# Kernel optimization log

Hardware: AMD Instinct MI355X
Metric: run time of the kernel (lower is better)

## Reference

```python
import jax, jax.numpy as jnp
import numpy as np

N = 50000       # nodes
E = 800000      # edges
IN = 256        # input channels
H = 4           # heads
C = 64          # hidden channels per head
NEG_SLOPE = 0.2 # PyG GATConv default LeakyReLU slope
EPS = 1e-16


def setup_inputs() -> dict:
    key = jax.random.key(0)
    k_x, k_e, k_w, k_as, k_ad = jax.random.split(key, 5)
    x = jax.random.normal(k_x, (N, IN), dtype=jnp.float32)
    edge_index = jax.random.randint(k_e, (2, E), 0, N, dtype=jnp.int64)
    # GATConv params: glorot-style scale
    W = jax.random.normal(k_w, (IN, H * C), dtype=jnp.float32) * (1.0 / np.sqrt(IN))
    att_src = jax.random.normal(k_as, (H, C), dtype=jnp.float32) * (1.0 / np.sqrt(C))
    att_dst = jax.random.normal(k_ad, (H, C), dtype=jnp.float32) * (1.0 / np.sqrt(C))
    return {"x": x, "edge_index": edge_index, "W": W, "att_src": att_src, "att_dst": att_dst}


def reference(x, edge_index, W, att_src, att_dst):
    src, dst = edge_index[0], edge_index[1]
    # linear projection, split heads: [N, H, C]
    xh = (x @ W).reshape(N, H, C)
    # per-node attention halves: [N, H]
    a_src = jnp.einsum('nhc,hc->nh', xh, att_src)
    a_dst = jnp.einsum('nhc,hc->nh', xh, att_dst)
    # per-edge logits with LeakyReLU: [E, H]
    alpha = a_src[src] + a_dst[dst]
    alpha = jnp.where(alpha >= 0, alpha, NEG_SLOPE * alpha)
    # segment softmax over destination nodes
    m = jax.ops.segment_max(alpha, dst, num_segments=N)          # [N, H]
    ex = jnp.exp(alpha - m[dst])                                  # [E, H]
    denom = jax.ops.segment_sum(ex, dst, num_segments=N)         # [N, H]
    att = ex / (denom[dst] + EPS)                                 # [E, H]
    # weighted message scatter-add: [N, H, C] -> concat heads [N, H*C]
    msg = att[:, :, None] * xh[src]                               # [E, H, C]
    out = jax.ops.segment_sum(msg, dst, num_segments=N)
    out = out.reshape(N, H * C)
    return (out, att)
```

## Files before the change

kernel.cpp:

```cpp
#include <hip/hip_runtime.h>
#include <math.h>

#define IN_CH   256
#define HC      256
#define H_HEADS 4
#define NEG_SLOPE 0.2f
#define LOG2E   1.44269504088896f
#define DEFER_THR 12.0f

typedef __attribute__((ext_vector_type(8))) short short8;
typedef __attribute__((ext_vector_type(4))) short short4v;
typedef __attribute__((ext_vector_type(4))) float float4v;

__device__ __forceinline__ float bf2f(unsigned short b) {
    return __uint_as_float(((unsigned)b) << 16);
}
__device__ __forceinline__ unsigned short f2bf(float f) {
    unsigned u = __float_as_uint(f);
    u += 0x7fffu + ((u >> 16) & 1u);
    return (unsigned short)(u >> 16);
}
__device__ __forceinline__ float lrelu(float a) {
    return a >= 0.f ? a : NEG_SLOPE * a;
}
__device__ __forceinline__ float fexp2(float a) {
    return __builtin_amdgcn_exp2f(a);
}


__global__ void prep_w(const float* __restrict__ w,
                       unsigned short* __restrict__ wt) {
    int idx = blockIdx.x * 256 + threadIdx.x;
    int k = idx >> 8, c = idx & 255;
    wt[(size_t)c * 256 + k] = f2bf(w[idx]);
}

__global__ __launch_bounds__(256) void gemm_xh(const float* __restrict__ x,
                                               const unsigned short* __restrict__ wt,
                                               const float* __restrict__ att_s,
                                               const float* __restrict__ att_d,
                                               unsigned short* __restrict__ xh_bf,
                                               float* __restrict__ a_src,
                                               float* __restrict__ a_dst, int N) {
    __shared__ __attribute__((aligned(16))) unsigned char lds_a[16384];
    int tid  = threadIdx.x;
    int wave = tid >> 6;
    int lane = tid & 63;
    int quad = lane >> 4;
    int l16  = lane & 15;
    int rb   = blockIdx.x * 16;

#pragma unroll
    for (int pass = 0; pass < 2; ++pass) {
        int s  = pass * 256 + tid;
        int kc = s >> 4;
        int m  = s & 15;
        int grow = rb + m; if (grow >= N) grow = N - 1;
        const float* gp = x + (size_t)grow * IN_CH + kc * 8;
        float4v f0 = *(const float4v*)gp;
        float4v f1 = *(const float4v*)(gp + 4);
        short8 hi, lo;
#pragma unroll
        for (int j = 0; j < 4; ++j) {
            unsigned short h0 = f2bf(f0[j]);
            hi[j] = (short)h0;
            lo[j] = (short)f2bf(f0[j] - bf2f(h0));
            unsigned short h1 = f2bf(f1[j]);
            hi[4 + j] = (short)h1;
            lo[4 + j] = (short)f2bf(f1[j] - bf2f(h1));
        }
        *(short8*)(lds_a + (size_t)s * 16) = hi;
        *(short8*)(lds_a + 8192 + (size_t)s * 16) = lo;
    }
    __syncthreads();

    float4v acc[4] = {};
    const unsigned short* wt_base = wt + ((size_t)wave * 64 + l16) * IN_CH;
#pragma unroll
    for (int k0 = 0; k0 < 8; ++k0) {
        int kc   = k0 * 4 + quad;
        int slot = kc * 16 + l16;
        short8 a_hi = *(const short8*)(lds_a + slot * 16);
        short8 a_lo = *(const short8*)(lds_a + 8192 + slot * 16);
#pragma unroll
        for (int ct = 0; ct < 4; ++ct) {
            short8 bh = *(const short8*)(wt_base + (size_t)ct * 16 * IN_CH
                                         + k0 * 32 + quad * 8);
            acc[ct] = __builtin_amdgcn_mfma_f32_16x16x32_bf16(a_lo, bh, acc[ct], 0, 0, 0);
            acc[ct] = __builtin_amdgcn_mfma_f32_16x16x32_bf16(a_hi, bh, acc[ct], 0, 0, 0);
        }
    }

    int cb = wave;
    float ps[4] = {0.f, 0.f, 0.f, 0.f};
    float pd[4] = {0.f, 0.f, 0.f, 0.f};
#pragma unroll
    for (int ct = 0; ct < 4; ++ct) {
        float as_c = att_s[cb * 64 + ct * 16 + l16] * LOG2E;
        float ad_c = att_d[cb * 64 + ct * 16 + l16] * LOG2E;
#pragma unroll
        for (int r = 0; r < 4; ++r) {
            float v = acc[ct][r];
            int grow = rb + quad * 4 + r;
            if (grow < N)
                xh_bf[(size_t)grow * HC + cb * 64 + ct * 16 + l16] = f2bf(v);
            ps[r] += v * as_c;
            pd[r] += v * ad_c;
        }
    }
#pragma unroll
    for (int off = 1; off < 16; off <<= 1) {
#pragma unroll
        for (int r = 0; r < 4; ++r) {
            ps[r] += __shfl_xor(ps[r], off);
            pd[r] += __shfl_xor(pd[r], off);
        }
    }
    if (l16 == 0) {
#pragma unroll
        for (int r = 0; r < 4; ++r) {
            int grow = rb + quad * 4 + r;
            if (grow < N) {
                a_src[(size_t)grow * 4 + cb] = ps[r];
                a_dst[(size_t)grow * 4 + cb] = pd[r];
            }
        }
    }
}

__global__ __launch_bounds__(256) void deg_count(const int* __restrict__ ei,
                                                 int* __restrict__ deg, int E) {
    int e = blockIdx.x * 256 + threadIdx.x;
    if (e >= E) return;
    atomicAdd(deg + ei[E + e], 1);
}


__global__ __launch_bounds__(256) void scan_part(const int* __restrict__ deg,
                                                 int* __restrict__ part, int N) {
    int t = threadIdx.x;
    int base = blockIdx.x * 1024 + t * 4;
    int s = 0;
    if (base + 4 <= N) {
        int4 v = *(const int4*)(deg + base);
        s = v.x + v.y + v.z + v.w;
    } else {
#pragma unroll
        for (int j = 0; j < 4; ++j)
            if (base + j < N) s += deg[base + j];
    }
#pragma unroll
    for (int off = 1; off < 64; off <<= 1) s += __shfl_xor(s, off);
    __shared__ int ws[4];
    if ((t & 63) == 0) ws[t >> 6] = s;
    __syncthreads();
    if (t == 0) part[blockIdx.x] = ws[0] + ws[1] + ws[2] + ws[3];
}

__global__ __launch_bounds__(256) void scan_final(const int* __restrict__ deg,
                                                  const int* __restrict__ part,
                                                  int* __restrict__ rowptr,
                                                  int* __restrict__ cursor, int N) {
    __shared__ int sm[256];
    __shared__ int wsum[4];
    int t = threadIdx.x;
    int bacc = 0;
    for (int j = t; j < blockIdx.x; j += 256) bacc += part[j];
#pragma unroll
    for (int off = 1; off < 64; off <<= 1) bacc += __shfl_xor(bacc, off);
    if ((t & 63) == 0) wsum[t >> 6] = bacc;

    int base = blockIdx.x * 1024 + t * 4;
    int v0 = 0, v1 = 0, v2 = 0, v3 = 0;
    if (base + 4 <= N) {
        int4 v = *(const int4*)(deg + base);
        v0 = v.x; v1 = v.y; v2 = v.z; v3 = v.w;
    } else {
        if (base + 0 < N) v0 = deg[base + 0];
        if (base + 1 < N) v1 = deg[base + 1];
        if (base + 2 < N) v2 = deg[base + 2];
        if (base + 3 < N) v3 = deg[base + 3];
    }
    int s = v0 + v1 + v2 + v3;
    sm[t] = s;
    __syncthreads();
    for (int off = 1; off < 256; off <<= 1) {
        int tmp = (t >= off) ? sm[t - off] : 0;
        __syncthreads();
        sm[t] += tmp;
        __syncthreads();
    }
    int boff = wsum[0] + wsum[1] + wsum[2] + wsum[3];
    int run = boff + sm[t] - s;
    int r0 = run, r1 = r0 + v0, r2 = r1 + v1, r3 = r2 + v2;
    if (base + 4 <= N) {
        *(int4*)(rowptr + base) = (int4){r0, r1, r2, r3};
        *(int4*)(cursor + base) = (int4){r0, r1, r2, r3};
    } else {
        if (base + 0 < N) { rowptr[base + 0] = r0; cursor[base + 0] = r0; }
        if (base + 1 < N) { rowptr[base + 1] = r1; cursor[base + 1] = r1; }
        if (base + 2 < N) { rowptr[base + 2] = r2; cursor[base + 2] = r2; }
        if (base + 3 < N) { rowptr[base + 3] = r3; cursor[base + 3] = r3; }
    }
}

__global__ __launch_bounds__(256) void fill_csr(const int* __restrict__ ei,
                                                int* __restrict__ cursor,
                                                int* __restrict__ csr_src, int E) {
    int e = blockIdx.x * 256 + threadIdx.x;
    if (e >= E) return;
    int s = ei[e], d = ei[E + e];
    int slot = atomicAdd(cursor + d, 1);
    csr_src[slot] = s;
}

__global__ __launch_bounds__(256) void gat_gather(const int* __restrict__ csr_src,
                                                  const int* __restrict__ rowptr,
                                                  const int* __restrict__ deg,
                                                  const float* __restrict__ a_src,
                                                  const float* __restrict__ a_dst,
                                                  const unsigned short* __restrict__ xh_bf,
                                                  float* __restrict__ out,
                                                  float* __restrict__ pack, int N) {
    int wave = threadIdx.x >> 6, lane = threadIdx.x & 63;
    int d = blockIdx.x * 4 + wave;
    if (d >= N) return;
    int h = lane >> 4;
    int start = rowptr[d], cnt = deg[d];
    float adst = a_dst[(size_t)d * 4 + h];

    if (cnt == 0) {
        *(float4v*)(out + (size_t)d * HC + lane * 4) = (float4v){0.f, 0.f, 0.f, 0.f};
        if ((lane & 15) == 0) {
            pack[(size_t)d * 12 + h]     = adst;
            pack[(size_t)d * 12 + 4 + h] = 0.f;
            pack[(size_t)d * 12 + 8 + h] = 0.f;
        }
        return;
    }

    float mE = -INFINITY, lE = 0.f, mO = -INFINITY, lO = 0.f;
    float4v accE = {0.f, 0.f, 0.f, 0.f}, accO = {0.f, 0.f, 0.f, 0.f};

    int s2 = 0, s3 = 0;
    float asE = 0.f, asO = 0.f;
    short4v xvE = {}, xvO = {};
    {
        int s0 = csr_src[start];
        asE = a_src[(size_t)s0 * 4 + h];
        xvE = *(const short4v*)(xh_bf + (size_t)s0 * HC + lane * 4);
    }
    if (cnt > 1) {
        int s1 = csr_src[start + 1];
        asO = a_src[(size_t)s1 * 4 + h];
        xvO = *(const short4v*)(xh_bf + (size_t)s1 * HC + lane * 4);
    }
    if (cnt > 2) s2 = csr_src[start + 2];
    if (cnt > 3) s3 = csr_src[start + 3];

    for (int i = 0; i < cnt; i += 2) {
        float asE_n = 0.f, asO_n = 0.f;
        short4v xvE_n = {}, xvO_n = {};
        if (i + 2 < cnt) {
            asE_n = a_src[(size_t)s2 * 4 + h];
            xvE_n = *(const short4v*)(xh_bf + (size_t)s2 * HC + lane * 4);
        }
        if (i + 3 < cnt) {
            asO_n = a_src[(size_t)s3 * 4 + h];
            xvO_n = *(const short4v*)(xh_bf + (size_t)s3 * HC + lane * 4);
        }
        int s4 = (i + 4 < cnt) ? csr_src[start + i + 4] : 0;
        int s5 = (i + 5 < cnt) ? csr_src[start + i + 5] : 0;

        bool haveO = (i + 1 < cnt);
        float alE = lrelu(asE + adst);
        bool ok = (alE <= mE + DEFER_THR);
        float alO = 0.f;
        if (haveO) {
            alO = lrelu(asO + adst);
            ok = ok && (alO <= mO + DEFER_THR);
        }
        if (__all(ok)) {
            float p = fexp2(alE - mE);
            lE += p;
#pragma unroll
            for (int j = 0; j < 4; ++j)
                accE[j] += p * bf2f((unsigned short)xvE[j]);
            if (haveO) {
                float q = fexp2(alO - mO);
                lO += q;
#pragma unroll
                for (int j = 0; j < 4; ++j)
                    accO[j] += q * bf2f((unsigned short)xvO[j]);
            }
        } else {
            {
                float mn = fmaxf(mE, alE);
                float sc = fexp2(mE - mn);
                float p  = fexp2(alE - mn);
                lE = lE * sc + p;
#pragma unroll
                for (int j = 0; j < 4; ++j)
                    accE[j] = accE[j] * sc + p * bf2f((unsigned short)xvE[j]);
                mE = mn;
            }
            if (haveO) {
                float mn = fmaxf(mO, alO);
                float sc = fexp2(mO - mn);
                float p  = fexp2(alO - mn);
                lO = lO * sc + p;
#pragma unroll
                for (int j = 0; j < 4; ++j)
                    accO[j] = accO[j] * sc + p * bf2f((unsigned short)xvO[j]);
                mO = mn;
            }
        }
        asE = asE_n; xvE = xvE_n; asO = asO_n; xvO = xvO_n;
        s2 = s4; s3 = s5;
    }
    float mm = fmaxf(mE, mO);
    float sE = fexp2(mE - mm), sO = fexp2(mO - mm);
    float l  = lE * sE + lO * sO;
    float inv = 1.f / (l + 1e-16f);
    float4v o;
#pragma unroll
    for (int j = 0; j < 4; ++j) o[j] = (accE[j] * sE + accO[j] * sO) * inv;
    *(float4v*)(out + (size_t)d * HC + lane * 4) = o;
    if ((lane & 15) == 0) {
        pack[(size_t)d * 12 + h]     = adst;
        pack[(size_t)d * 12 + 4 + h] = mm;
        pack[(size_t)d * 12 + 8 + h] = inv;
    }
}

__global__ __launch_bounds__(256) void att_edge(const int* __restrict__ ei,
                                                const float* __restrict__ a_src,
                                                const float* __restrict__ pack,
                                                float* __restrict__ att_out, int E) {
    int e = blockIdx.x * 256 + threadIdx.x;
    if (e >= E) return;
    int s = ei[e], d = ei[E + e];
    float4v as = *(const float4v*)(a_src + (size_t)s * 4);
    float4v ad = *(const float4v*)(pack + (size_t)d * 12);
    float4v mm = *(const float4v*)(pack + (size_t)d * 12 + 4);
    float4v gg = *(const float4v*)(pack + (size_t)d * 12 + 8);
    float4v o;
#pragma unroll
    for (int h = 0; h < 4; ++h)
        o[h] = fexp2(lrelu(as[h] + ad[h]) - mm[h]) * gg[h];
    *(float4v*)(att_out + (size_t)e * 4) = o;
}

extern "C" void kernel_launch(void* const* d_in, const int* in_sizes, int n_in,
                              void* d_out, int out_size, void* d_ws, size_t ws_size,
                              hipStream_t stream) {
    const float* x     = (const float*)d_in[0];
    const int*   ei    = (const int*)d_in[1];
    const float* W     = (const float*)d_in[2];
    const float* att_s = (const float*)d_in[3];
    const float* att_d = (const float*)d_in[4];

    const int N = in_sizes[0] / IN_CH;
    const int E = in_sizes[1] / 2;

    char* ws = (char*)d_ws;
    size_t off = 0;
    unsigned short* xh_bf = (unsigned short*)(ws + off); off += (size_t)N * HC * 2;
    unsigned short* wt    = (unsigned short*)(ws + off); off += (size_t)IN_CH * HC * 2;
    float* a_src = (float*)(ws + off); off += (size_t)N * H_HEADS * 4;
    float* a_dst = (float*)(ws + off); off += (size_t)N * H_HEADS * 4;
    float* pack  = (float*)(ws + off); off += (size_t)N * 12 * 4;
    int* rowptr  = (int*)(ws + off); off += (size_t)N * 4;
    int* cursor  = (int*)(ws + off); off += (size_t)N * 4;
    int* csr_src = (int*)(ws + off); off += (size_t)E * 4;
    int* part    = (int*)(ws + off); off += 1024 * 4;
    size_t zoff = off;
    int* deg     = (int*)(ws + off); off += (size_t)N * 4;

    float* out     = (float*)d_out;
    float* out_att = out + (size_t)N * HC;

    (void)hipMemsetAsync(ws + zoff, 0, off - zoff, stream);

    const int NB = (N + 1023) / 1024;

    prep_w<<<256, 256, 0, stream>>>(W, wt);
    deg_count<<<(E + 255) / 256, 256, 0, stream>>>(ei, deg, E);
    gemm_xh<<<(N + 15) / 16, 256, 0, stream>>>(x, wt, att_s, att_d,
                                               xh_bf, a_src, a_dst, N);
    scan_part<<<NB, 256, 0, stream>>>(deg, part, N);
    scan_final<<<NB, 256, 0, stream>>>(deg, part, rowptr, cursor, N);
    fill_csr<<<(E + 255) / 256, 256, 0, stream>>>(ei, cursor, csr_src, E);
    gat_gather<<<(N + 3) / 4, 256, 0, stream>>>(csr_src, rowptr, deg, a_src, a_dst,
                                                xh_bf, out, pack, N);
    att_edge<<<(E + 255) / 256, 256, 0, stream>>>(ei, a_src, pack, out_att, E);
}
```

Before: 332.1 us.

## Precompute per-edge LeakyReLU logits during CSR fill and store in CSR and edge order

fill_csr now gathers a_src[s] and a_dst[d], computes the four per-head LeakyReLU logits and writes them both in CSR slot order (csr_al) and in original edge order (al_e). gat_gather reads logits contiguously from csr_al instead of randomly gathering a_src per neighbor, and att_edge reads al_e instead of gathering a_src and a_dst. This swaps random gathers in the later kernels for extra writes of two E×4 float arrays (about 25 MB) and a scattered store in fill_csr, which may offset the savings.

```diff
diff --git a/kernel.cpp b/kernel.cpp
--- a/kernel.cpp
+++ b/kernel.cpp
@@ -205,20 +205,30 @@
 }
 
 __global__ __launch_bounds__(256) void fill_csr(const int* __restrict__ ei,
+                                                const float* __restrict__ a_src,
+                                                const float* __restrict__ a_dst,
                                                 int* __restrict__ cursor,
-                                                int* __restrict__ csr_src, int E) {
+                                                int* __restrict__ csr_src,
+                                                float* __restrict__ csr_al,
+                                                float* __restrict__ al_e, int E) {
     int e = blockIdx.x * 256 + threadIdx.x;
     if (e >= E) return;
     int s = ei[e], d = ei[E + e];
+    float4v as = *(const float4v*)(a_src + (size_t)s * 4);
+    float4v ad = *(const float4v*)(a_dst + (size_t)d * 4);
+    float4v al;
+#pragma unroll
+    for (int h = 0; h < 4; ++h) al[h] = lrelu(as[h] + ad[h]);
     int slot = atomicAdd(cursor + d, 1);
     csr_src[slot] = s;
+    *(float4v*)(csr_al + (size_t)slot * 4) = al;
+    *(float4v*)(al_e + (size_t)e * 4) = al;
 }
 
 __global__ __launch_bounds__(256) void gat_gather(const int* __restrict__ csr_src,
+                                                  const float* __restrict__ csr_al,
                                                   const int* __restrict__ rowptr,
                                                   const int* __restrict__ deg,
-                                                  const float* __restrict__ a_src,
-                                                  const float* __restrict__ a_dst,
                                                   const unsigned short* __restrict__ xh_bf,
                                                   float* __restrict__ out,
                                                   float* __restrict__ pack, int N) {
@@ -227,14 +237,12 @@
     if (d >= N) return;
     int h = lane >> 4;
     int start = rowptr[d], cnt = deg[d];
-    float adst = a_dst[(size_t)d * 4 + h];
 
     if (cnt == 0) {
         *(float4v*)(out + (size_t)d * HC + lane * 4) = (float4v){0.f, 0.f, 0.f, 0.f};
         if ((lane & 15) == 0) {
-            pack[(size_t)d * 12 + h]     = adst;
-            pack[(size_t)d * 12 + 4 + h] = 0.f;
-            pack[(size_t)d * 12 + 8 + h] = 0.f;
+            pack[(size_t)d * 8 + h]     = 0.f;
+            pack[(size_t)d * 8 + 4 + h] = 0.f;
         }
         return;
     }
@@ -243,43 +251,38 @@
     float4v accE = {0.f, 0.f, 0.f, 0.f}, accO = {0.f, 0.f, 0.f, 0.f};
 
     int s2 = 0, s3 = 0;
-    float asE = 0.f, asO = 0.f;
+    float alE = 0.f, alO = 0.f;
     short4v xvE = {}, xvO = {};
     {
         int s0 = csr_src[start];
-        asE = a_src[(size_t)s0 * 4 + h];
+        alE = csr_al[(size_t)start * 4 + h];
         xvE = *(const short4v*)(xh_bf + (size_t)s0 * HC + lane * 4);
     }
     if (cnt > 1) {
         int s1 = csr_src[start + 1];
-        asO = a_src[(size_t)s1 * 4 + h];
+        alO = csr_al[(size_t)(start + 1) * 4 + h];
         xvO = *(const short4v*)(xh_bf + (size_t)s1 * HC + lane * 4);
     }
     if (cnt > 2) s2 = csr_src[start + 2];
     if (cnt > 3) s3 = csr_src[start + 3];
 
     for (int i = 0; i < cnt; i += 2) {
-        float asE_n = 0.f, asO_n = 0.f;
+        float alE_n = 0.f, alO_n = 0.f;
         short4v xvE_n = {}, xvO_n = {};
         if (i + 2 < cnt) {
-            asE_n = a_src[(size_t)s2 * 4 + h];
+            alE_n = csr_al[(size_t)(start + i + 2) * 4 + h];
             xvE_n = *(const short4v*)(xh_bf + (size_t)s2 * HC + lane * 4);
         }
         if (i + 3 < cnt) {
-            asO_n = a_src[(size_t)s3 * 4 + h];
+            alO_n = csr_al[(size_t)(start + i + 3) * 4 + h];
             xvO_n = *(const short4v*)(xh_bf + (size_t)s3 * HC + lane * 4);
         }
         int s4 = (i + 4 < cnt) ? csr_src[start + i + 4] : 0;
         int s5 = (i + 5 < cnt) ? csr_src[start + i + 5] : 0;
 
         bool haveO = (i + 1 < cnt);
-        float alE = lrelu(asE + adst);
         bool ok = (alE <= mE + DEFER_THR);
-        float alO = 0.f;
-        if (haveO) {
-            alO = lrelu(asO + adst);
-            ok = ok && (alO <= mO + DEFER_THR);
-        }
+        if (haveO) ok = ok && (alO <= mO + DEFER_THR);
         if (__all(ok)) {
             float p = fexp2(alE - mE);
             lE += p;
@@ -315,7 +318,7 @@
                 mO = mn;
             }
         }
-        asE = asE_n; xvE = xvE_n; asO = asO_n; xvO = xvO_n;
+        alE = alE_n; xvE = xvE_n; alO = alO_n; xvO = xvO_n;
         s2 = s4; s3 = s5;
     }
     float mm = fmaxf(mE, mO);
@@ -327,27 +330,25 @@
     for (int j = 0; j < 4; ++j) o[j] = (accE[j] * sE + accO[j] * sO) * inv;
     *(float4v*)(out + (size_t)d * HC + lane * 4) = o;
     if ((lane & 15) == 0) {
-        pack[(size_t)d * 12 + h]     = adst;
-        pack[(size_t)d * 12 + 4 + h] = mm;
-        pack[(size_t)d * 12 + 8 + h] = inv;
+        pack[(size_t)d * 8 + h]     = mm;
+        pack[(size_t)d * 8 + 4 + h] = inv;
     }
 }
 
 __global__ __launch_bounds__(256) void att_edge(const int* __restrict__ ei,
-                                                const float* __restrict__ a_src,
+                                                const float* __restrict__ al_e,
                                                 const float* __restrict__ pack,
                                                 float* __restrict__ att_out, int E) {
     int e = blockIdx.x * 256 + threadIdx.x;
     if (e >= E) return;
-    int s = ei[e], d = ei[E + e];
-    float4v as = *(const float4v*)(a_src + (size_t)s * 4);
-    float4v ad = *(const float4v*)(pack + (size_t)d * 12);
-    float4v mm = *(const float4v*)(pack + (size_t)d * 12 + 4);
-    float4v gg = *(const float4v*)(pack + (size_t)d * 12 + 8);
+    int d = ei[E + e];
+    float4v al = *(const float4v*)(al_e + (size_t)e * 4);
+    float4v mm = *(const float4v*)(pack + (size_t)d * 8);
+    float4v gg = *(const float4v*)(pack + (size_t)d * 8 + 4);
     float4v o;
 #pragma unroll
     for (int h = 0; h < 4; ++h)
-        o[h] = fexp2(lrelu(as[h] + ad[h]) - mm[h]) * gg[h];
+        o[h] = fexp2(al[h] - mm[h]) * gg[h];
     *(float4v*)(att_out + (size_t)e * 4) = o;
 }
 
@@ -369,10 +370,12 @@
     unsigned short* wt    = (unsigned short*)(ws + off); off += (size_t)IN_CH * HC * 2;
     float* a_src = (float*)(ws + off); off += (size_t)N * H_HEADS * 4;
     float* a_dst = (float*)(ws + off); off += (size_t)N * H_HEADS * 4;
-    float* pack  = (float*)(ws + off); off += (size_t)N * 12 * 4;
+    float* pack  = (float*)(ws + off); off += (size_t)N * 8 * 4;
     int* rowptr  = (int*)(ws + off); off += (size_t)N * 4;
     int* cursor  = (int*)(ws + off); off += (size_t)N * 4;
     int* csr_src = (int*)(ws + off); off += (size_t)E * 4;
+    float* csr_al = (float*)(ws + off); off += (size_t)E * 4 * 4;
+    float* al_e   = (float*)(ws + off); off += (size_t)E * 4 * 4;
     int* part    = (int*)(ws + off); off += 1024 * 4;
     size_t zoff = off;
     int* deg     = (int*)(ws + off); off += (size_t)N * 4;
@@ -390,8 +393,9 @@
                                                xh_bf, a_src, a_dst, N);
     scan_part<<<NB, 256, 0, stream>>>(deg, part, N);
     scan_final<<<NB, 256, 0, stream>>>(deg, part, rowptr, cursor, N);
-    fill_csr<<<(E + 255) / 256, 256, 0, stream>>>(ei, cursor, csr_src, E);
-    gat_gather<<<(N + 3) / 4, 256, 0, stream>>>(csr_src, rowptr, deg, a_src, a_dst,
+    fill_csr<<<(E + 255) / 256, 256, 0, stream>>>(ei, a_src, a_dst, cursor,
+                                                  csr_src, csr_al, al_e, E);
+    gat_gather<<<(N + 3) / 4, 256, 0, stream>>>(csr_src, csr_al, rowptr, deg,
                                                 xh_bf, out, pack, N);
-    att_edge<<<(E + 255) / 256, 256, 0, stream>>>(ei, a_src, pack, out_att, E);
-}
+    att_edge<<<(E + 255) / 256, 256, 0, stream>>>(ei, al_e, pack, out_att, E);
+}
```

Measured after the change: 324.2 us. 1.02x faster.
